# Optimization experiments

Measured on AMD Instinct MI355X. Metric: run time of the kernel, lower is better.

The kernel has to match this reference:

```python
import jax, jax.numpy as jnp
import numpy as np

DIM = 1024
N_HEADS = 16
HEAD_DIM = DIM // N_HEADS
SCALE = 1.0 / HEAD_DIM ** 0.5


def setup_inputs() -> dict:
    key = jax.random.key(0)
    k1, k2, k3, k4, k5 = jax.random.split(key, 5)
    B, T = 4, 2048
    x = jax.random.normal(k1, (B, T, DIM), dtype=jnp.float32)
    # torch nn.Linear weights: y = x @ W.T + b
    w_qkv = jax.random.normal(k2, (3 * DIM, DIM), dtype=jnp.float32) * 0.02
    b_qkv = jax.random.normal(k3, (3 * DIM,), dtype=jnp.float32) * 0.02
    w_proj = jax.random.normal(k4, (DIM, DIM), dtype=jnp.float32) * 0.02
    b_proj = jax.random.normal(k5, (DIM,), dtype=jnp.float32) * 0.02
    return {"x": x, "w_qkv": w_qkv, "b_qkv": b_qkv, "w_proj": w_proj, "b_proj": b_proj}


def reference(x, w_qkv, b_qkv, w_proj, b_proj):
    B, T, D = x.shape
    qkv = x @ w_qkv.T + b_qkv                              # [B, T, 3D]
    qkv = qkv.reshape(B, T, 3, N_HEADS, HEAD_DIM)
    qkv = jnp.transpose(qkv, (2, 0, 3, 1, 4))              # [3, B, h, T, d]
    q, k, v = qkv[0], qkv[1], qkv[2]
    s = jnp.einsum('bhqd,bhkd->bhqk', q, k) * SCALE        # [B, h, T, T]
    attn = jax.nn.softmax(s, axis=-1)
    out = jnp.einsum('bhqk,bhkd->bqhd', attn, v)           # [B, T, h, d]
    out = out.reshape(B, T, D)
    return out @ w_proj.T + b_proj
```

## Files before the change

### kernel.cpp

```cpp
#include <hip/hip_runtime.h>
#include <stdint.h>

typedef short short8 __attribute__((ext_vector_type(8)));
typedef _Float16 half4 __attribute__((ext_vector_type(4)));
typedef _Float16 half8 __attribute__((ext_vector_type(8)));
typedef __fp16 fp16x2 __attribute__((ext_vector_type(2)));
typedef unsigned int uint2v __attribute__((ext_vector_type(2)));
typedef unsigned int uintx4 __attribute__((ext_vector_type(4)));
typedef float floatx4 __attribute__((ext_vector_type(4)));

#define LOG2E 1.44269504088896340736f
#define QSCALE (0.125f * LOG2E)

static __device__ __forceinline__ unsigned short f2bf(float f) {
  unsigned int u = __float_as_uint(f);
  u += 0x7fffu + ((u >> 16) & 1u);
  return (unsigned short)(u >> 16);
}

static __device__ __forceinline__ float fexp2(float x) {
#if __has_builtin(__builtin_amdgcn_exp2f)
  return __builtin_amdgcn_exp2f(x);
#else
  return exp2f(x);
#endif
}

#define GLD_LDS16(gp, lp)                                                      \
  __builtin_amdgcn_global_load_lds(                                            \
      (const __attribute__((address_space(1))) void*)(gp),                     \
      (__attribute__((address_space(3))) void*)(lp), 16, 0, 0)

__global__ __launch_bounds__(256) void cvt_f32_bf16(
    const float* __restrict__ in, unsigned short* __restrict__ out, int n) {
  int i = (blockIdx.x * 256 + threadIdx.x) * 4;
  if (i >= n) return;
  float4 v = *(const float4*)(in + i);
  ushort4 u;
  u.x = f2bf(v.x); u.y = f2bf(v.y); u.z = f2bf(v.z); u.w = f2bf(v.w);
  *(ushort4*)(out + i) = u;
}

template <int MODE>
__global__ __launch_bounds__(256, 4) void gemm_bt(
    const unsigned short* __restrict__ A, const unsigned short* __restrict__ Bm,
    const float* __restrict__ bias, float* __restrict__ outF,
    unsigned short* __restrict__ qo, unsigned short* __restrict__ ko,
    _Float16* __restrict__ vto, int M, int N, int K) {
  __shared__ unsigned short As[128 * 64];
  __shared__ unsigned short Bs[128 * 64];
  const int tid = threadIdx.x;
  const int w = tid >> 6, l = tid & 63;
  const int lr = l & 15, lg = l >> 4;
  const int nbn = N >> 7;
  const int nwg = gridDim.x;
  const int bid = blockIdx.x;
  const int cpx = nwg >> 3;
  const int swz = (bid & 7) * cpx + (bid >> 3);
  const int bm = swz / nbn, bn = swz % nbn;
  const int wm = w >> 1, wn = w & 1;

  floatx4 acc[4][4];
#pragma unroll
  for (int i = 0; i < 4; ++i)
#pragma unroll
    for (int j = 0; j < 4; ++j) acc[i][j] = (floatx4){0.f, 0.f, 0.f, 0.f};

  const int sw0 = ((0 * 4 + lg) ^ (lr & 7)) * 8;
  const int sw1 = ((1 * 4 + lg) ^ (lr & 7)) * 8;

  for (int k0 = 0; k0 < K; k0 += 64) {
#pragma unroll
    for (int i = 0; i < 4; ++i) {
      int c = i * 256 + tid;
      int row = c >> 3, sl = (c & 7) ^ (row & 7);
      const unsigned short* ga =
          A + ((size_t)bm * 128 + row) * K + k0 + sl * 8;
      GLD_LDS16(ga, As + (size_t)(i * 256 + w * 64) * 8);
    }
#pragma unroll
    for (int i = 0; i < 4; ++i) {
      int c = i * 256 + tid;
      int row = c >> 3, sl = (c & 7) ^ (row & 7);
      const unsigned short* gb =
          Bm + ((size_t)bn * 128 + row) * K + k0 + sl * 8;
      GLD_LDS16(gb, Bs + (size_t)(i * 256 + w * 64) * 8);
    }
    __syncthreads();
#pragma unroll
    for (int kk = 0; kk < 2; ++kk) {
      const int sw = kk ? sw1 : sw0;
      short8 af[4], bf[4];
#pragma unroll
      for (int i = 0; i < 4; ++i)
        af[i] = *(const short8*)&As[(wm * 64 + i * 16 + lr) * 64 + sw];
#pragma unroll
      for (int j = 0; j < 4; ++j)
        bf[j] = *(const short8*)&Bs[(wn * 64 + j * 16 + lr) * 64 + sw];
#pragma unroll
      for (int i = 0; i < 4; ++i)
#pragma unroll
        for (int j = 0; j < 4; ++j)
          acc[i][j] = __builtin_amdgcn_mfma_f32_16x16x32_bf16(af[i], bf[j],
                                                              acc[i][j], 0, 0, 0);
    }
    __syncthreads();
  }

#pragma unroll
  for (int i = 0; i < 4; ++i) {
    int row0 = bm * 128 + wm * 64 + i * 16 + lg * 4;
#pragma unroll
    for (int j = 0; j < 4; ++j) {
      int col = bn * 128 + wn * 64 + j * 16 + lr;
      float bv = bias[col];
#pragma unroll
      for (int jj = 0; jj < 4; ++jj) {
        float v = acc[i][j][jj] + bv;
        int r = row0 + jj;
        if (MODE == 0) {
          outF[(size_t)r * N + col] = v;
        } else {
          int three = col >> 10, cc = col & 1023;
          int h = cc >> 6, d = cc & 63;
          int b = r >> 11, t = r & 2047;
          if (three == 0)
            qo[(((size_t)(b * 16 + h)) * 2048 + t) * 64 + d] = f2bf(v * QSCALE);
          else if (three == 1)
            ko[(((size_t)(b * 16 + h)) * 2048 + t) * 64 + d] = f2bf(v);
          else
            vto[(((size_t)(b * 16 + h)) * 64 + d) * 2048 + t] = (_Float16)v;
        }
      }
    }
  }
}

__global__ __launch_bounds__(256, 3) void attn_fwd(
    const unsigned short* __restrict__ Qg, const unsigned short* __restrict__ Kg,
    const _Float16* __restrict__ VTg, unsigned short* __restrict__ Og) {
  __shared__ unsigned short Ks[2][64 * 64];
  __shared__ _Float16 Vs[2][64 * 64];

  const int bid0 = blockIdx.x;
  const int bid = (bid0 & 7) * 128 + (bid0 >> 3);
  const int bh = bid >> 4, qt = bid & 15;
  const int b = bh >> 4, hh = bh & 15;
  const int tid = threadIdx.x, w = tid >> 6, l = tid & 63;
  const int l4 = l & 15, g = l >> 4;
  const unsigned short* Q = Qg + (size_t)bh * (2048 * 64);
  const unsigned short* Kp = Kg + (size_t)bh * (2048 * 64);
  const _Float16* VT = VTg + (size_t)bh * (64 * 2048);
  const int qw = qt * 128 + w * 32;

  const int r0 = tid >> 3;
  const int s0 = (tid & 7) ^ (r0 & 7);
  const int kv0 = (r0 & 16) ? (((r0 & 15) >> 2) * 8 + 4 + (r0 & 3))
                            : ((r0 >> 2) * 8 + (r0 & 3));
  const unsigned short* kp0 = Kp + (size_t)kv0 * 64 + s0 * 8;
  const unsigned short* kp1 = Kp + (size_t)(kv0 + 32) * 64 + s0 * 8;
  const _Float16* vp0 = VT + (size_t)r0 * 2048 + s0 * 8;
  const _Float16* vp1 = VT + (size_t)(r0 + 32) * 2048 + s0 * 8;
  unsigned short* ksd0 = &Ks[0][tid * 8];
  unsigned short* ksd1 = &Ks[0][(256 + tid) * 8];
  _Float16* vsd0 = &Vs[0][tid * 8];
  _Float16* vsd1 = &Vs[0][(256 + tid) * 8];

#define STAGE(bufofs, tt)                                                     \
  do {                                                                        \
    GLD_LDS16(kp0 + (size_t)(tt) * 64, ksd0 + (bufofs) * 4096);               \
    GLD_LDS16(kp1 + (size_t)(tt) * 64, ksd1 + (bufofs) * 4096);               \
    GLD_LDS16(vp0 + (tt), vsd0 + (bufofs) * 4096);                            \
    GLD_LDS16(vp1 + (tt), vsd1 + (bufofs) * 4096);                            \
  } while (0)

  const int kb0 = l4 * 64 + ((g ^ (l4 & 7)) * 8);
  const int kb1 = l4 * 64 + (((4 + g) ^ (l4 & 7)) * 8);
  int vb[2];
#pragma unroll
  for (int B = 0; B < 2; ++B)
    vb[B] = l4 * 64 + (((B * 4 + g) ^ (l4 & 7)) * 8);

  short8 qf[2][2];
#pragma unroll
  for (int qs = 0; qs < 2; ++qs)
#pragma unroll
    for (int c = 0; c < 2; ++c)
      qf[qs][c] =
          *(const short8*)&Q[(size_t)(qw + qs * 16 + l4) * 64 + c * 32 + g * 8];

  floatx4 o[2][4];
#pragma unroll
  for (int qs = 0; qs < 2; ++qs)
#pragma unroll
    for (int db = 0; db < 4; ++db) o[qs][db] = (floatx4){0.f, 0.f, 0.f, 0.f};
  float m[2] = {-__builtin_inff(), -__builtin_inff()};
  float lp[2] = {0.f, 0.f};

  STAGE(0, 0);
  __syncthreads();

#pragma unroll 2
  for (int it = 0; it < 32; ++it) {
    const int cur = it & 1;
    if (it + 1 < 32) STAGE(cur ^ 1, (it + 1) * 64);

    floatx4 s[2][4];
#pragma unroll
    for (int f = 0; f < 4; ++f) {
      short8 kf0 = *(const short8*)&Ks[cur][kb0 + f * 1024];
      short8 kf1 = *(const short8*)&Ks[cur][kb1 + f * 1024];
      floatx4 z = (floatx4){0.f, 0.f, 0.f, 0.f};
      floatx4 t00 = __builtin_amdgcn_mfma_f32_16x16x32_bf16(kf0, qf[0][0], z, 0, 0, 0);
      s[0][f] = __builtin_amdgcn_mfma_f32_16x16x32_bf16(kf1, qf[0][1], t00, 0, 0, 0);
      floatx4 t10 = __builtin_amdgcn_mfma_f32_16x16x32_bf16(kf0, qf[1][0], z, 0, 0, 0);
      s[1][f] = __builtin_amdgcn_mfma_f32_16x16x32_bf16(kf1, qf[1][1], t10, 0, 0, 0);
    }

    uint2v pu[2][4];
#pragma unroll
    for (int qs = 0; qs < 2; ++qs) {
      float e[16];
      float rs = 0.f;
#pragma unroll
      for (int f = 0; f < 4; ++f)
#pragma unroll
        for (int jj = 0; jj < 4; ++jj) {
          float pv = fexp2(s[qs][f][jj] - m[qs]);
          e[f * 4 + jj] = pv;
          rs += pv;
        }

      if (!__all(rs <= 256.0f)) {
        float a0 = fmaxf(fmaxf(s[qs][0][0], s[qs][0][1]), fmaxf(s[qs][0][2], s[qs][0][3]));
        float a1 = fmaxf(fmaxf(s[qs][1][0], s[qs][1][1]), fmaxf(s[qs][1][2], s[qs][1][3]));
        float a2 = fmaxf(fmaxf(s[qs][2][0], s[qs][2][1]), fmaxf(s[qs][2][2], s[qs][2][3]));
        float a3 = fmaxf(fmaxf(s[qs][3][0], s[qs][3][1]), fmaxf(s[qs][3][2], s[qs][3][3]));
        float pp = fmaxf(fmaxf(a0, a1), fmaxf(a2, a3));
        pp = fmaxf(pp, __shfl_xor(pp, 16));
        pp = fmaxf(pp, __shfl_xor(pp, 32));
        float mo = m[qs];
        m[qs] = fmaxf(mo, pp);
        float al = fexp2(mo - m[qs]);
        lp[qs] *= al;
#pragma unroll
        for (int jj = 0; jj < 4; ++jj) {
          float alr = __shfl(al, g * 4 + jj);
          o[qs][0][jj] *= alr; o[qs][1][jj] *= alr;
          o[qs][2][jj] *= alr; o[qs][3][jj] *= alr;
        }
        rs = 0.f;
#pragma unroll
        for (int f = 0; f < 4; ++f)
#pragma unroll
          for (int jj = 0; jj < 4; ++jj) {
            float pv = fexp2(s[qs][f][jj] - m[qs]);
            e[f * 4 + jj] = pv;
            rs += pv;
          }
      }
      lp[qs] += rs;

#pragma unroll
      for (int f = 0; f < 4; ++f) {
        fp16x2 plo = __builtin_amdgcn_cvt_pkrtz(e[f * 4 + 0], e[f * 4 + 1]);
        fp16x2 phi = __builtin_amdgcn_cvt_pkrtz(e[f * 4 + 2], e[f * 4 + 3]);
        pu[qs][f].x = __builtin_bit_cast(unsigned int, plo);
        pu[qs][f].y = __builtin_bit_cast(unsigned int, phi);
      }
    }

#pragma unroll
    for (int B = 0; B < 2; ++B) {
      uintx4 ua0, ua1;
      ua0.x = pu[0][2 * B].x;     ua0.y = pu[0][2 * B].y;
      ua0.z = pu[0][2 * B + 1].x; ua0.w = pu[0][2 * B + 1].y;
      ua1.x = pu[1][2 * B].x;     ua1.y = pu[1][2 * B].y;
      ua1.z = pu[1][2 * B + 1].x; ua1.w = pu[1][2 * B + 1].y;
      half8 pa0 = __builtin_bit_cast(half8, ua0);
      half8 pa1 = __builtin_bit_cast(half8, ua1);
#pragma unroll
      for (int db = 0; db < 4; ++db) {
        half8 vf = *(const half8*)&Vs[cur][vb[B] + db * 1024];
        o[0][db] = __builtin_amdgcn_mfma_f32_16x16x32_f16(pa0, vf, o[0][db], 0, 0, 0);
        o[1][db] = __builtin_amdgcn_mfma_f32_16x16x32_f16(pa1, vf, o[1][db], 0, 0, 0);
      }
    }
    __syncthreads();
  }

#pragma unroll
  for (int qs = 0; qs < 2; ++qs) {
    float ls = lp[qs];
    ls += __shfl_xor(ls, 16);
    ls += __shfl_xor(ls, 32);
    float invq = 1.f / ls;
    float inv[4];
#pragma unroll
    for (int jj = 0; jj < 4; ++jj) inv[jj] = __shfl(invq, g * 4 + jj);
#pragma unroll
    for (int db = 0; db < 4; ++db)
#pragma unroll
      for (int jj = 0; jj < 4; ++jj)
        Og[((size_t)b * 2048 + qw + qs * 16 + g * 4 + jj) * 1024 + hh * 64 +
           db * 16 + l4] = f2bf(o[qs][db][jj] * inv[jj]);
  }
#undef STAGE
}

extern "C" void kernel_launch(void* const* d_in, const int* in_sizes, int n_in,
                              void* d_out, int out_size, void* d_ws, size_t ws_size,
                              hipStream_t stream) {
  const float* x = (const float*)d_in[0];
  const float* w_qkv = (const float*)d_in[1];
  const float* b_qkv = (const float*)d_in[2];
  const float* w_proj = (const float*)d_in[3];
  const float* b_proj = (const float*)d_in[4];
  float* out = (float*)d_out;

  char* p = (char*)d_ws;
  unsigned short* xb = (unsigned short*)p;     p += (size_t)8192 * 1024 * 2;
  unsigned short* wqkvb = (unsigned short*)p;  p += (size_t)3072 * 1024 * 2;
  unsigned short* wprojb = (unsigned short*)p; p += (size_t)1024 * 1024 * 2;
  unsigned short* qb = (unsigned short*)p;     p += (size_t)64 * 2048 * 64 * 2;
  unsigned short* kb = (unsigned short*)p;     p += (size_t)64 * 2048 * 64 * 2;
  _Float16* vtb = (_Float16*)p;                p += (size_t)64 * 64 * 2048 * 2;
  unsigned short* attnb = (unsigned short*)p;  p += (size_t)8192 * 1024 * 2;

  cvt_f32_bf16<<<dim3(8192), dim3(256), 0, stream>>>(x, xb, 8192 * 1024);
  cvt_f32_bf16<<<dim3(3072), dim3(256), 0, stream>>>(w_qkv, wqkvb, 3072 * 1024);
  cvt_f32_bf16<<<dim3(1024), dim3(256), 0, stream>>>(w_proj, wprojb, 1024 * 1024);

  gemm_bt<1><<<dim3(64 * 24), dim3(256), 0, stream>>>(
      xb, wqkvb, b_qkv, nullptr, qb, kb, vtb, 8192, 3072, 1024);

  attn_fwd<<<dim3(1024), dim3(256), 0, stream>>>(qb, kb, vtb, attnb);

  gemm_bt<0><<<dim3(64 * 8), dim3(256), 0, stream>>>(
      attnb, wprojb, b_proj, out, nullptr, nullptr, nullptr, 8192, 1024, 1024);
}
```

Measured before the change: 197.4 us.

## Fold max subtraction into MFMA accumulator and compute row sums via MFMA

The running max is now applied by seeding the QK^T MFMA accumulator with -m, so exp2 is taken directly on the scores without a separate subtraction. The rescale test now uses a lazy max threshold, triggering only when a score exceeds 8. The per-lane row-sum accumulation and its final cross-lane shuffles are replaced by an extra MFMA that multiplies P by a ones vector, producing row sums already in the output layout. s_setprio hints are also added around the MFMA blocks. This removes VALU adds and shuffles at the cost of extra MFMA work, and the fp16 P values now feed the sum directly.

New measurement: 197.1 us. No clear change (-0.2%).

```diff
diff --git a/kernel.cpp b/kernel.cpp
--- a/kernel.cpp
+++ b/kernel.cpp
@@ -189,13 +189,17 @@
       qf[qs][c] =
           *(const short8*)&Q[(size_t)(qw + qs * 16 + l4) * 64 + c * 32 + g * 8];
 
+  half8 onesv;
+#pragma unroll
+  for (int e = 0; e < 8; ++e) onesv[e] = (_Float16)1.0f;
+
   floatx4 o[2][4];
 #pragma unroll
   for (int qs = 0; qs < 2; ++qs)
 #pragma unroll
     for (int db = 0; db < 4; ++db) o[qs][db] = (floatx4){0.f, 0.f, 0.f, 0.f};
-  float m[2] = {-__builtin_inff(), -__builtin_inff()};
-  float lp[2] = {0.f, 0.f};
+  floatx4 osum[2] = {(floatx4){0.f, 0.f, 0.f, 0.f}, (floatx4){0.f, 0.f, 0.f, 0.f}};
+  float m[2] = {0.f, 0.f};
 
   STAGE(0, 0);
   __syncthreads();
@@ -206,60 +210,54 @@
     if (it + 1 < 32) STAGE(cur ^ 1, (it + 1) * 64);
 
     floatx4 s[2][4];
+    const floatx4 i0 = (floatx4){-m[0], -m[0], -m[0], -m[0]};
+    const floatx4 i1 = (floatx4){-m[1], -m[1], -m[1], -m[1]};
+    __builtin_amdgcn_s_setprio(1);
 #pragma unroll
     for (int f = 0; f < 4; ++f) {
       short8 kf0 = *(const short8*)&Ks[cur][kb0 + f * 1024];
       short8 kf1 = *(const short8*)&Ks[cur][kb1 + f * 1024];
-      floatx4 z = (floatx4){0.f, 0.f, 0.f, 0.f};
-      floatx4 t00 = __builtin_amdgcn_mfma_f32_16x16x32_bf16(kf0, qf[0][0], z, 0, 0, 0);
+      floatx4 t00 = __builtin_amdgcn_mfma_f32_16x16x32_bf16(kf0, qf[0][0], i0, 0, 0, 0);
       s[0][f] = __builtin_amdgcn_mfma_f32_16x16x32_bf16(kf1, qf[0][1], t00, 0, 0, 0);
-      floatx4 t10 = __builtin_amdgcn_mfma_f32_16x16x32_bf16(kf0, qf[1][0], z, 0, 0, 0);
+      floatx4 t10 = __builtin_amdgcn_mfma_f32_16x16x32_bf16(kf0, qf[1][0], i1, 0, 0, 0);
       s[1][f] = __builtin_amdgcn_mfma_f32_16x16x32_bf16(kf1, qf[1][1], t10, 0, 0, 0);
     }
+    __builtin_amdgcn_s_setprio(0);
 
     uint2v pu[2][4];
 #pragma unroll
     for (int qs = 0; qs < 2; ++qs) {
       float e[16];
-      float rs = 0.f;
 #pragma unroll
       for (int f = 0; f < 4; ++f)
 #pragma unroll
-        for (int jj = 0; jj < 4; ++jj) {
-          float pv = fexp2(s[qs][f][jj] - m[qs]);
-          e[f * 4 + jj] = pv;
-          rs += pv;
-        }
-
-      if (!__all(rs <= 256.0f)) {
-        float a0 = fmaxf(fmaxf(s[qs][0][0], s[qs][0][1]), fmaxf(s[qs][0][2], s[qs][0][3]));
-        float a1 = fmaxf(fmaxf(s[qs][1][0], s[qs][1][1]), fmaxf(s[qs][1][2], s[qs][1][3]));
-        float a2 = fmaxf(fmaxf(s[qs][2][0], s[qs][2][1]), fmaxf(s[qs][2][2], s[qs][2][3]));
-        float a3 = fmaxf(fmaxf(s[qs][3][0], s[qs][3][1]), fmaxf(s[qs][3][2], s[qs][3][3]));
-        float pp = fmaxf(fmaxf(a0, a1), fmaxf(a2, a3));
-        pp = fmaxf(pp, __shfl_xor(pp, 16));
-        pp = fmaxf(pp, __shfl_xor(pp, 32));
-        float mo = m[qs];
-        m[qs] = fmaxf(mo, pp);
-        float al = fexp2(mo - m[qs]);
-        lp[qs] *= al;
+        for (int jj = 0; jj < 4; ++jj) e[f * 4 + jj] = fexp2(s[qs][f][jj]);
+
+      float p01 = fmaxf(fmaxf(s[qs][0][0], s[qs][0][1]), fmaxf(s[qs][0][2], s[qs][0][3]));
+      float p23 = fmaxf(fmaxf(s[qs][1][0], s[qs][1][1]), fmaxf(s[qs][1][2], s[qs][1][3]));
+      float p45 = fmaxf(fmaxf(s[qs][2][0], s[qs][2][1]), fmaxf(s[qs][2][2], s[qs][2][3]));
+      float p67 = fmaxf(fmaxf(s[qs][3][0], s[qs][3][1]), fmaxf(s[qs][3][2], s[qs][3][3]));
+      float pp = fmaxf(fmaxf(p01, p23), fmaxf(p45, p67));
+
+      if (!__all(pp <= 8.0f)) {
+        float pm = fmaxf(pp, __shfl_xor(pp, 16));
+        pm = fmaxf(pm, __shfl_xor(pm, 32));
+        float dm = fmaxf(pm, 0.0f);
+        m[qs] += dm;
+        float al = fexp2(-dm);
 #pragma unroll
         for (int jj = 0; jj < 4; ++jj) {
           float alr = __shfl(al, g * 4 + jj);
           o[qs][0][jj] *= alr; o[qs][1][jj] *= alr;
           o[qs][2][jj] *= alr; o[qs][3][jj] *= alr;
+          osum[qs][jj] *= alr;
         }
-        rs = 0.f;
 #pragma unroll
         for (int f = 0; f < 4; ++f)
 #pragma unroll
-          for (int jj = 0; jj < 4; ++jj) {
-            float pv = fexp2(s[qs][f][jj] - m[qs]);
-            e[f * 4 + jj] = pv;
-            rs += pv;
-          }
+          for (int jj = 0; jj < 4; ++jj)
+            e[f * 4 + jj] = fexp2(s[qs][f][jj] - dm);
       }
-      lp[qs] += rs;
 
 #pragma unroll
       for (int f = 0; f < 4; ++f) {
@@ -270,6 +268,7 @@
       }
     }
 
+    __builtin_amdgcn_s_setprio(1);
 #pragma unroll
     for (int B = 0; B < 2; ++B) {
       uintx4 ua0, ua1;
@@ -279,6 +278,8 @@
       ua1.z = pu[1][2 * B + 1].x; ua1.w = pu[1][2 * B + 1].y;
       half8 pa0 = __builtin_bit_cast(half8, ua0);
       half8 pa1 = __builtin_bit_cast(half8, ua1);
+      osum[0] = __builtin_amdgcn_mfma_f32_16x16x32_f16(pa0, onesv, osum[0], 0, 0, 0);
+      osum[1] = __builtin_amdgcn_mfma_f32_16x16x32_f16(pa1, onesv, osum[1], 0, 0, 0);
 #pragma unroll
       for (int db = 0; db < 4; ++db) {
         half8 vf = *(const half8*)&Vs[cur][vb[B] + db * 1024];
@@ -286,18 +287,15 @@
         o[1][db] = __builtin_amdgcn_mfma_f32_16x16x32_f16(pa1, vf, o[1][db], 0, 0, 0);
       }
     }
+    __builtin_amdgcn_s_setprio(0);
     __syncthreads();
   }
 
 #pragma unroll
   for (int qs = 0; qs < 2; ++qs) {
-    float ls = lp[qs];
-    ls += __shfl_xor(ls, 16);
-    ls += __shfl_xor(ls, 32);
-    float invq = 1.f / ls;
     float inv[4];
 #pragma unroll
-    for (int jj = 0; jj < 4; ++jj) inv[jj] = __shfl(invq, g * 4 + jj);
+    for (int jj = 0; jj < 4; ++jj) inv[jj] = 1.f / osum[qs][jj];
 #pragma unroll
     for (int db = 0; db < 4; ++db)
 #pragma unroll
```
